# Optimization experiments

Hardware: AMD Instinct MI355X
Metric: run time of the kernel (lower is better)

The kernel has to match this reference:

```python
import jax, jax.numpy as jnp
import numpy as np

B, S, D = 2, 1024, 4096
HQ, HKV, HD = 32, 8, 128
GROUPS = HQ // HKV          # 4
SCALE = HD ** -0.5


def _rope_tables(key):
    # standard RoPE cos/sin tables, non-interleaved (half-split) layout
    inv_freq = 1.0 / (10000.0 ** (jnp.arange(0, HD, 2, dtype=jnp.float32) / HD))  # [HD/2]
    pos = jnp.arange(S, dtype=jnp.float32)                                        # [S]
    freqs = pos[:, None] * inv_freq[None, :]                                      # [S, HD/2]
    emb = jnp.concatenate([freqs, freqs], axis=-1)                                # [S, HD]
    cos = jnp.broadcast_to(jnp.cos(emb)[None], (B, S, HD))
    sin = jnp.broadcast_to(jnp.sin(emb)[None], (B, S, HD))
    return cos, sin


def setup_inputs() -> dict:
    key = jax.random.key(0)
    ks = jax.random.split(key, 6)
    hidden_states = jax.random.normal(ks[0], (B, S, D), dtype=jnp.float32)
    cos_table, sin_table = _rope_tables(ks[1])
    Wq = jax.random.normal(ks[2], (D, HQ * HD), dtype=jnp.float32) * (D ** -0.5)
    Wk = jax.random.normal(ks[3], (D, HKV * HD), dtype=jnp.float32) * (D ** -0.5)
    Wv = jax.random.normal(ks[4], (D, HKV * HD), dtype=jnp.float32) * (D ** -0.5)
    Wo = jax.random.normal(ks[5], (HQ * HD, D), dtype=jnp.float32) * ((HQ * HD) ** -0.5)
    return {"hidden_states": hidden_states, "cos_table": cos_table,
            "sin_table": sin_table, "Wq": Wq, "Wk": Wk, "Wv": Wv, "Wo": Wo}


def _rotate_half(x):
    x1, x2 = jnp.split(x, 2, axis=-1)
    return jnp.concatenate([-x2, x1], axis=-1)


def _apply_rope(x, cos, sin):
    # x: [B, S, H, HD]; cos/sin: [B, S, HD] broadcast across heads
    c = cos[:, :, None, :]
    s = sin[:, :, None, :]
    return x * c + _rotate_half(x) * s


def reference(hidden_states, cos_table, sin_table, Wq, Wk, Wv, Wo):
    b, s, _ = hidden_states.shape
    # QKV projections (no bias, Llama-style)
    q = (hidden_states @ Wq).reshape(b, s, HQ, HD)
    k = (hidden_states @ Wk).reshape(b, s, HKV, HD)
    v = (hidden_states @ Wv).reshape(b, s, HKV, HD)
    # fused RoPE on q and k (in [B, S, H, HD] layout, as in source)
    q = _apply_rope(q, cos_table, sin_table)
    k = _apply_rope(k, cos_table, sin_table)
    # -> [B, H, S, HD]
    q = q.transpose(0, 2, 1, 3)
    k = k.transpose(0, 2, 1, 3)
    v = v.transpose(0, 2, 1, 3)
    # GQA repeat_kv: [B, HKV, S, HD] -> [B, HQ, S, HD]
    k = jnp.repeat(k, GROUPS, axis=1)
    v = jnp.repeat(v, GROUPS, axis=1)
    # SDPA, no mask (source calls sdpa without a mask)
    scores = jnp.einsum('bhqd,bhkd->bhqk', q, k) * SCALE
    attn = jax.nn.softmax(scores, axis=-1)
    out = jnp.einsum('bhqk,bhkd->bhqd', attn, v)
    out = out.transpose(0, 2, 1, 3).reshape(b, s, HQ * HD)
    return out @ Wo
```

## Files before the change

kernel.cpp:

```cpp
#include <hip/hip_runtime.h>

#define B_   2
#define S_   1024
#define D_   4096
#define HQ_  32
#define HKV_ 8
#define HD_  128
#define SCALE_ 0.08838834764831845f

typedef unsigned short u16;
typedef __attribute__((ext_vector_type(8))) short s16x8;
typedef __attribute__((ext_vector_type(4))) short s16x4;
typedef __attribute__((ext_vector_type(4))) float f32x4;

#define MFMA(a,b,c) __builtin_amdgcn_mfma_f32_16x16x32_bf16((a),(b),(c),0,0,0)

__device__ __forceinline__ u16 bf16_rne(float x) {
  unsigned u = __float_as_uint(x);
  u += 0x7fffu + ((u >> 16) & 1u);
  return (u16)(u >> 16);
}
__device__ __forceinline__ float bf16_up(u16 h) {
  return __uint_as_float(((unsigned)h) << 16);
}
__device__ __forceinline__ void split2(float x, u16& h, u16& l) {
  h = bf16_rne(x);
  l = bf16_rne(x - bf16_up(h));
}

__device__ __forceinline__ void cvt_hi_lo(float a, float b, unsigned& hi, unsigned& lo) {
  unsigned h, l;
  asm("v_cvt_pk_bf16_f32 %0, %1, %2" : "=v"(h) : "v"(a), "v"(b));
  float ra = __uint_as_float(h << 16);
  float rb = __uint_as_float(h & 0xffff0000u);
  float la = a - ra, lb = b - rb;
  asm("v_cvt_pk_bf16_f32 %0, %1, %2" : "=v"(l) : "v"(la), "v"(lb));
  hi = h; lo = l;
}
__device__ __forceinline__ void pack8(float4 x, float4 y, uint4& h, uint4& l) {
  unsigned h0,h1,h2,h3,l0,l1,l2,l3;
  cvt_hi_lo(x.x, x.y, h0, l0);
  cvt_hi_lo(x.z, x.w, h1, l1);
  cvt_hi_lo(y.x, y.y, h2, l2);
  cvt_hi_lo(y.z, y.w, h3, l3);
  h = make_uint4(h0,h1,h2,h3); l = make_uint4(l0,l1,l2,l3);
}

typedef const __attribute__((address_space(1))) void* gas_ptr;
typedef __attribute__((address_space(3))) void* las_ptr;
__device__ __forceinline__ void gload_lds16(const void* g, void* l) {
  __builtin_amdgcn_global_load_lds((gas_ptr)g, (las_ptr)l, 16, 0, 0);
}

__global__ __launch_bounds__(256) void frag_b1(
    const float* __restrict__ W, u16* __restrict__ dh, u16* __restrict__ dl,
    int N, int n0, int Nc16)
{
  __shared__ float T[32][68];
  const int kt = blockIdx.x, nbk = blockIdx.y;
  const int tid = threadIdx.x;
#pragma unroll
  for (int rep = 0; rep < 2; ++rep) {
    int idx = tid + rep * 256;
    int row = idx >> 4, c4 = (idx & 15) * 4;
    float4 v = *reinterpret_cast<const float4*>(&W[(size_t)(kt*32 + row) * N + n0 + nbk*64 + c4]);
    *reinterpret_cast<float4*>(&T[row][c4]) = v;
  }
  __syncthreads();
  const size_t base = ((size_t)kt * Nc16 + nbk * 4) * 512;
  int c = tid;
  int nt = c >> 6, l = c & 63, kc = l >> 4, r = l & 15;
  u16 hh[8], ll[8];
#pragma unroll
  for (int j = 0; j < 8; ++j) split2(T[kc*8 + j][nt*16 + r], hh[j], ll[j]);
  *reinterpret_cast<s16x8*>(&dh[base + (size_t)c * 8]) =
    (s16x8){(short)hh[0],(short)hh[1],(short)hh[2],(short)hh[3],
            (short)hh[4],(short)hh[5],(short)hh[6],(short)hh[7]};
  *reinterpret_cast<s16x8*>(&dl[base + (size_t)c * 8]) =
    (s16x8){(short)ll[0],(short)ll[1],(short)ll[2],(short)ll[3],
            (short)ll[4],(short)ll[5],(short)ll[6],(short)ll[7]};
}

__global__ __launch_bounds__(256) void frag_b2(
    const float* __restrict__ W, u16* __restrict__ dh, u16* __restrict__ dl,
    int N, int n0, int Nc16)
{
  __shared__ float T[32][68];
  const int kt = blockIdx.x, nbk = blockIdx.y;
  const int tid = threadIdx.x;
#pragma unroll
  for (int rep = 0; rep < 2; ++rep) {
    int idx = tid + rep * 256;
    int row = idx >> 4, c4 = (idx & 15) * 4;
    float4 v = *reinterpret_cast<const float4*>(&W[(size_t)(kt*32 + row) * N + n0 + nbk*64 + c4]);
    *reinterpret_cast<float4*>(&T[row][c4]) = v;
  }
  __syncthreads();
  int c = tid;
  int nt = c >> 6, l = c & 63;
  const size_t base = (((size_t)(kt >> 1) * Nc16 + nbk*4 + nt) * 2 + (kt & 1)) * 512;
  u16 hh[8], ll[8];
#pragma unroll
  for (int j = 0; j < 8; ++j) split2(T[(l >> 4)*8 + j][nt*16 + (l & 15)], hh[j], ll[j]);
  *reinterpret_cast<s16x8*>(&dh[base + (size_t)l * 8]) =
    (s16x8){(short)hh[0],(short)hh[1],(short)hh[2],(short)hh[3],
            (short)hh[4],(short)hh[5],(short)hh[6],(short)hh[7]};
  *reinterpret_cast<s16x8*>(&dl[base + (size_t)l * 8]) =
    (s16x8){(short)ll[0],(short)ll[1],(short)ll[2],(short)ll[3],
            (short)ll[4],(short)ll[5],(short)ll[6],(short)ll[7]};
}

__global__ __launch_bounds__(256) void frag_a(
    const float* __restrict__ src, u16* __restrict__ dh, u16* __restrict__ dl)
{
  __shared__ float T[128][68];
  const int kt = blockIdx.x;
  const int mb = blockIdx.y;
  const int tid = threadIdx.x;
#pragma unroll
  for (int rep = 0; rep < 8; ++rep) {
    int idx = tid + rep * 256;
    int row = idx >> 4, c4 = (idx & 15) * 4;
    float4 v = *reinterpret_cast<const float4*>(&src[(size_t)(mb*128 + row) * 4096 + kt*64 + c4]);
    *reinterpret_cast<float4*>(&T[row][c4]) = v;
  }
  __syncthreads();
#pragma unroll
  for (int rep = 0; rep < 4; ++rep) {
    int c = tid + rep * 256;
    int mt = c >> 7, rem = c & 127, kk = rem >> 6, l = rem & 63;
    u16 hh[8], ll[8];
#pragma unroll
    for (int j = 0; j < 8; ++j)
      split2(T[mt*16 + (l & 15)][kk*32 + (l >> 4)*8 + j], hh[j], ll[j]);
    size_t off = (((size_t)(kt*128 + mb*8 + mt)) * 2 + kk) * 512 + (size_t)l * 8;
    *reinterpret_cast<s16x8*>(&dh[off]) =
      (s16x8){(short)hh[0],(short)hh[1],(short)hh[2],(short)hh[3],
              (short)hh[4],(short)hh[5],(short)hh[6],(short)hh[7]};
    *reinterpret_cast<s16x8*>(&dl[off]) =
      (s16x8){(short)ll[0],(short)ll[1],(short)ll[2],(short)ll[3],
              (short)ll[4],(short)ll[5],(short)ll[6],(short)ll[7]};
  }
}

__device__ __forceinline__ void gemm256_core(
    const u16* __restrict__ PAh, const u16* __restrict__ PAl,
    const u16* __restrict__ PBh, const u16* __restrict__ PBl,
    float* __restrict__ C, int ldc, int Nc16,
    int mb, int nb, int vk0, int nvk, u16* L)
{
  const int tid  = threadIdx.x;
  const int lane = tid & 63;
  const int wid  = tid >> 6;
  const int loff = lane * 8;
  const int wm8  = (wid >> 2) * 8;
  const int wn4  = (wid & 3) * 4;

  f32x4 acc[8][4];
#pragma unroll
  for (int i = 0; i < 8; ++i)
#pragma unroll
    for (int j = 0; j < 4; ++j) acc[i][j] = (f32x4){0.f,0.f,0.f,0.f};

  const size_t aBase = (size_t)mb * 16384;
  const size_t bBase = (size_t)nb * 16384;

#define STAGE256(v, la_, lb_)                                                  \
  {                                                                            \
    int p_ = (v) >> 6, vk_ = (v) & 63;                                         \
    const u16* sa_ = ((p_ == 1) ? PAl : PAh) + (size_t)vk_ * 131072 + aBase;   \
    const u16* sb_ = ((p_ == 2) ? PBl : PBh) + (size_t)vk_ * ((size_t)Nc16 * 1024) + bBase; \
    _Pragma("unroll")                                                          \
    for (int s_ = 0; s_ < 4; ++s_) {                                           \
      int ch_ = wid * 4 + s_;                                                  \
      gload_lds16(sa_ + ch_*512 + loff, (la_) + ch_*512);                      \
      gload_lds16(sb_ + ch_*512 + loff, (lb_) + ch_*512);                      \
    }                                                                          \
  }

  {
    u16* la = L + ((vk0 & 1) ? 16384 : 0);
    u16* lb = L + 32768 + ((vk0 & 1) ? 16384 : 0);
    STAGE256(vk0, la, lb);
  }
  __syncthreads();

  for (int t = vk0; t < vk0 + nvk; ++t) {
    u16* la = L + ((t & 1) ? 16384 : 0);
    u16* lb = L + 32768 + ((t & 1) ? 16384 : 0);
    if (t + 1 < vk0 + nvk) {
      u16* na = L + (((t+1) & 1) ? 16384 : 0);
      u16* nbuf = L + 32768 + (((t+1) & 1) ? 16384 : 0);
      STAGE256(t+1, na, nbuf);
    }
#pragma unroll
    for (int kk = 0; kk < 2; ++kk) {
      s16x8 a[8];
#pragma unroll
      for (int mf = 0; mf < 8; ++mf)
        a[mf] = *reinterpret_cast<const s16x8*>(&la[((wm8+mf)*2 + kk)*512 + loff]);
      __builtin_amdgcn_s_setprio(1);
#pragma unroll
      for (int nf = 0; nf < 4; ++nf) {
        s16x8 b = *reinterpret_cast<const s16x8*>(&lb[((wn4+nf)*2 + kk)*512 + loff]);
#pragma unroll
        for (int mf = 0; mf < 8; ++mf)
          acc[mf][nf] = MFMA(a[mf], b, acc[mf][nf]);
      }
      __builtin_amdgcn_s_setprio(0);
    }
    __syncthreads();
  }
#undef STAGE256

  const int lg = lane >> 4, lr = lane & 15;
  const int row0 = mb*256 + (wid >> 2) * 128;
  const int col0 = nb*256 + (wid & 3) * 64;
#pragma unroll
  for (int mf = 0; mf < 8; ++mf)
#pragma unroll
    for (int nf = 0; nf < 4; ++nf)
#pragma unroll
      for (int r = 0; r < 4; ++r)
        C[(size_t)(row0 + mf*16 + lg*4 + r) * ldc + col0 + nf*16 + lr] = acc[mf][nf][r];
}

__global__ __launch_bounds__(512) void gemm_qkv2(
    const u16* __restrict__ XAh, const u16* __restrict__ XAl,
    const u16* __restrict__ WA,
    float* __restrict__ qb, float* __restrict__ kb, float* __restrict__ vb)
{
  __shared__ __attribute__((aligned(16))) u16 L[65536];
  int id = blockIdx.x;
  int swz = (id & 7) * 24 + (id >> 3);
  const u16 *Bh, *Bl; float* C; int ldc, Nc16, mb, nb;
  if (swz < 128)      { Bh = WA;          Bl = WA+16777216; C = qb; ldc = 4096; Nc16 = 256; mb = swz & 7;  nb = swz >> 3; }
  else if (swz < 160) { int u = swz-128; Bh = WA+33554432; Bl = WA+37748736; C = kb; ldc = 1024; Nc16 = 64; mb = u & 7; nb = u >> 3; }
  else                { int u = swz-160; Bh = WA+41943040; Bl = WA+46137344; C = vb; ldc = 1024; Nc16 = 64; mb = u & 7; nb = u >> 3; }
  gemm256_core(XAh, XAl, Bh, Bl, C, ldc, Nc16, mb, nb, 0, 192, L);
}

__global__ __launch_bounds__(512) void gemm_out2(
    const u16* __restrict__ ABh, const u16* __restrict__ ABl,
    const u16* __restrict__ WOh, const u16* __restrict__ WOl,
    float* __restrict__ outp, float* __restrict__ c2)
{
  __shared__ __attribute__((aligned(16))) u16 L[65536];
  int id = blockIdx.x;
  int swz = (id & 7) * 32 + (id >> 3);
  int u = swz & 127, s = swz >> 7;
  int mb = u & 7, nb = u >> 3;
  gemm256_core(ABh, ABl, WOh, WOl, s ? c2 : outp, 4096, 256, mb, nb, s*96, 96, L);
}

__global__ __launch_bounds__(256) void add_out(
    float* __restrict__ o, const float* __restrict__ c2)
{
  int i = blockIdx.x * 256 + threadIdx.x;
  float4 a = reinterpret_cast<float4*>(o)[i];
  float4 b = reinterpret_cast<const float4*>(c2)[i];
  a.x += b.x; a.y += b.y; a.z += b.z; a.w += b.w;
  reinterpret_cast<float4*>(o)[i] = a;
}

__global__ __launch_bounds__(256) void frag_kv(
    const float* __restrict__ kb, const float* __restrict__ vb,
    const float* __restrict__ cosT, const float* __restrict__ sinT,
    u16* __restrict__ KFh, u16* __restrict__ KFl,
    u16* __restrict__ VFh, u16* __restrict__ VFl)
{
  __shared__ float T[32][132];
  const int bid  = blockIdx.x;
  const int isV  = bid >> 9;
  const int bkvh = (bid >> 5) & 15;
  const int chnk = bid & 31;
  const int tid  = threadIdx.x;
  const int b    = bkvh >> 3, kvh = bkvh & 7;

  const float* src = isV ? vb : kb;
  {
    int r0 = tid >> 5, c4 = (tid & 31) * 4;
    float sgn = (c4 < 64) ? -1.f : 1.f;
#pragma unroll
    for (int it = 0; it < 4; ++it) {
      int row = r0 + it * 8;
      int srow = chnk*32 + row;
      const float* rp = &src[(((size_t)(b * S_ + srow)) * HKV_ + kvh) * HD_];
      float4 v = *reinterpret_cast<const float4*>(rp + c4);
      if (!isV) {
        float4 p  = *reinterpret_cast<const float4*>(rp + (c4 ^ 64));
        float4 cc = *reinterpret_cast<const float4*>(&cosT[((size_t)(b*S_ + srow))*HD_ + c4]);
        float4 ss = *reinterpret_cast<const float4*>(&sinT[((size_t)(b*S_ + srow))*HD_ + c4]);
        v.x = v.x*cc.x + sgn*p.x*ss.x;
        v.y = v.y*cc.y + sgn*p.y*ss.y;
        v.z = v.z*cc.z + sgn*p.z*ss.z;
        v.w = v.w*cc.w + sgn*p.w*ss.w;
      }
      *reinterpret_cast<float4*>(&T[row][c4]) = v;
    }
  }
  __syncthreads();
#pragma unroll
  for (int rep = 0; rep < 2; ++rep) {
    int c2 = tid + rep * 256;
    int l = c2 & 63;
    u16 hh[8], ll[8];
    if (!isV) {
      int f = c2 >> 6, st_loc = f >> 2, dt = f & 3;
#pragma unroll
      for (int j = 0; j < 8; ++j)
        split2(T[st_loc*16 + (l & 15)][dt*32 + (l >> 4)*8 + j], hh[j], ll[j]);
      size_t off = ((size_t)bkvh*64 + chnk*2) * 2048 + (size_t)c2 * 8;
      *reinterpret_cast<s16x8*>(&KFh[off]) =
        (s16x8){(short)hh[0],(short)hh[1],(short)hh[2],(short)hh[3],
                (short)hh[4],(short)hh[5],(short)hh[6],(short)hh[7]};
      *reinterpret_cast<s16x8*>(&KFl[off]) =
        (s16x8){(short)ll[0],(short)ll[1],(short)ll[2],(short)ll[3],
                (short)ll[4],(short)ll[5],(short)ll[6],(short)ll[7]};
    } else {
      int dt16 = c2 >> 6;
#pragma unroll
      for (int j = 0; j < 8; ++j)
        split2(T[(l >> 4)*8 + j][dt16*16 + (l & 15)], hh[j], ll[j]);
      size_t off = ((size_t)bkvh*32 + chnk) * 4096 + (size_t)c2 * 8;
      *reinterpret_cast<s16x8*>(&VFh[off]) =
        (s16x8){(short)hh[0],(short)hh[1],(short)hh[2],(short)hh[3],
                (short)hh[4],(short)hh[5],(short)hh[6],(short)hh[7]};
      *reinterpret_cast<s16x8*>(&VFl[off]) =
        (s16x8){(short)ll[0],(short)ll[1],(short)ll[2],(short)ll[3],
                (short)ll[4],(short)ll[5],(short)ll[6],(short)ll[7]};
    }
  }
}

__global__ __launch_bounds__(512) void attn3(
    const float* __restrict__ qb,
    const float* __restrict__ cosT, const float* __restrict__ sinT,
    const u16* __restrict__ KFh, const u16* __restrict__ KFl,
    const u16* __restrict__ VFh, const u16* __restrict__ VFl,
    float* __restrict__ ob)
{
  __shared__ __attribute__((aligned(16))) u16 Klds[16384];
  __shared__ __attribute__((aligned(16))) u16 Vlds[16384];
  __shared__ u16 Ph[8][16][68], Pl[8][16][68];

  const int tid  = threadIdx.x;
  const int lane = tid & 63;
  const int wid  = tid >> 6;
  const int lr   = lane & 15;
  const int lg   = lane >> 4;
  const int loff = lane * 8;
  const int qt   = blockIdx.x;
  const int bh   = blockIdx.y;
  const int b    = bh >> 5, h = bh & 31;
  const int bkvh = b * 8 + (h >> 2);

  s16x8 qh[4], ql[4];
  {
    const int qrow = qt * 128 + wid * 16 + lr;
    const float* qp = qb + ((size_t)((b * S_ + qrow) * HQ_ + h)) * HD_;
    const float* cp = cosT + ((size_t)(b * S_ + qrow)) * HD_;
    const float* sp = sinT + ((size_t)(b * S_ + qrow)) * HD_;
#pragma unroll
    for (int kc = 0; kc < 4; ++kc) {
      const int d0 = kc * 32 + lg * 8;
      const float sgn = (d0 < 64) ? -1.f : 1.f;
      float4 v0 = *reinterpret_cast<const float4*>(qp + d0);
      float4 v1 = *reinterpret_cast<const float4*>(qp + d0 + 4);
      float4 p0 = *reinterpret_cast<const float4*>(qp + (d0 ^ 64));
      float4 p1 = *reinterpret_cast<const float4*>(qp + (d0 ^ 64) + 4);
      float4 c0 = *reinterpret_cast<const float4*>(cp + d0);
      float4 c1 = *reinterpret_cast<const float4*>(cp + d0 + 4);
      float4 s0 = *reinterpret_cast<const float4*>(sp + d0);
      float4 s1 = *reinterpret_cast<const float4*>(sp + d0 + 4);
      float4 r0, r1;
      r0.x = v0.x*c0.x + sgn*p0.x*s0.x;  r0.y = v0.y*c0.y + sgn*p0.y*s0.y;
      r0.z = v0.z*c0.z + sgn*p0.z*s0.z;  r0.w = v0.w*c0.w + sgn*p0.w*s0.w;
      r1.x = v1.x*c1.x + sgn*p1.x*s1.x;  r1.y = v1.y*c1.y + sgn*p1.y*s1.y;
      r1.z = v1.z*c1.z + sgn*p1.z*s1.z;  r1.w = v1.w*c1.w + sgn*p1.w*s1.w;
      uint4 h4, l4; pack8(r0, r1, h4, l4);
      qh[kc] = *reinterpret_cast<s16x8*>(&h4);
      ql[kc] = *reinterpret_cast<s16x8*>(&l4);
    }
  }

  f32x4 acc_o[8];
#pragma unroll
  for (int df = 0; df < 8; ++df) acc_o[df] = (f32x4){0.f, 0.f, 0.f, 0.f};
  float m_run[4] = {-1e30f, -1e30f, -1e30f, -1e30f};
  float l_run[4] = {0.f, 0.f, 0.f, 0.f};

  const u16* gKh = KFh + (size_t)bkvh * 131072;
  const u16* gKl = KFl + (size_t)bkvh * 131072;
  const u16* gVh = VFh + (size_t)bkvh * 131072;
  const u16* gVl = VFl + (size_t)bkvh * 131072;

#pragma unroll
  for (int i = 0; i < 4; ++i) {
    int idx = wid * 4 + i;
    const u16* src = (idx < 16) ? (gKh + idx*512) : (gKl + (idx-16)*512);
    u16* dst = Klds + ((idx < 16) ? idx*512 : 8192 + (idx-16)*512);
    gload_lds16(src + loff, dst);
  }
  __syncthreads();

  for (int t = 0; t < 16; ++t) {
#pragma unroll
    for (int i = 0; i < 4; ++i) {
      int idx = wid * 4 + i;
      const u16* src = (idx < 16) ? (gVh + t*8192 + idx*512)
                                  : (gVl + t*8192 + (idx-16)*512);
      u16* dst = Vlds + ((idx < 16) ? idx*512 : 8192 + (idx-16)*512);
      gload_lds16(src + loff, dst);
    }

    f32x4 accs[4];
#pragma unroll
    for (int nf = 0; nf < 4; ++nf) {
      accs[nf] = (f32x4){0.f, 0.f, 0.f, 0.f};
      s16x8 kh8[4], kl8[4];
#pragma unroll
      for (int kc = 0; kc < 4; ++kc) {
        kh8[kc] = *reinterpret_cast<const s16x8*>(&Klds[nf*2048 + kc*512 + loff]);
        kl8[kc] = *reinterpret_cast<const s16x8*>(&Klds[8192 + nf*2048 + kc*512 + loff]);
      }
#pragma unroll
      for (int kc = 0; kc < 4; ++kc) {
        accs[nf] = MFMA(qh[kc], kh8[kc], accs[nf]);
        accs[nf] = MFMA(ql[kc], kh8[kc], accs[nf]);
        accs[nf] = MFMA(qh[kc], kl8[kc], accs[nf]);
      }
    }
#pragma unroll
    for (int nf = 0; nf < 4; ++nf) accs[nf] *= SCALE_;

    float corr[4], rsum[4];
#pragma unroll
    for (int r = 0; r < 4; ++r) {
      float t0 = fmaxf(fmaxf(accs[0][r], accs[1][r]), fmaxf(accs[2][r], accs[3][r]));
      t0 = fmaxf(t0, __shfl_xor(t0, 1));
      t0 = fmaxf(t0, __shfl_xor(t0, 2));
      t0 = fmaxf(t0, __shfl_xor(t0, 4));
      t0 = fmaxf(t0, __shfl_xor(t0, 8));
      float mnew = fmaxf(m_run[r], t0);
      corr[r] = __expf(m_run[r] - mnew);
      m_run[r] = mnew;
      rsum[r] = 0.f;
    }
#pragma unroll
    for (int nf = 0; nf < 4; ++nf)
#pragma unroll
      for (int r = 0; r < 4; ++r) {
        float p = __expf(accs[nf][r] - m_run[r]);
        rsum[r] += p;
        u16 ph, pl;
        split2(p, ph, pl);
        Ph[wid][lg*4 + r][nf*16 + lr] = ph;
        Pl[wid][lg*4 + r][nf*16 + lr] = pl;
      }
#pragma unroll
    for (int r = 0; r < 4; ++r) {
      float s = rsum[r];
      s += __shfl_xor(s, 1); s += __shfl_xor(s, 2);
      s += __shfl_xor(s, 4); s += __shfl_xor(s, 8);
      l_run[r] = l_run[r] * corr[r] + s;
    }
#pragma unroll
    for (int df = 0; df < 8; ++df)
#pragma unroll
      for (int r = 0; r < 4; ++r) acc_o[df][r] *= corr[r];

    __syncthreads();

    if (t < 15) {
#pragma unroll
      for (int i = 0; i < 4; ++i) {
        int idx = wid * 4 + i;
        const u16* src = (idx < 16) ? (gKh + (t+1)*8192 + idx*512)
                                    : (gKl + (t+1)*8192 + (idx-16)*512);
        u16* dst = Klds + ((idx < 16) ? idx*512 : 8192 + (idx-16)*512);
        gload_lds16(src + loff, dst);
      }
    }

    s16x8 pa_h[2], pa_l[2];
#pragma unroll
    for (int kc = 0; kc < 2; ++kc) {
      pa_h[kc] = *reinterpret_cast<const s16x8*>(&Ph[wid][lr][kc*32 + lg*8]);
      pa_l[kc] = *reinterpret_cast<const s16x8*>(&Pl[wid][lr][kc*32 + lg*8]);
    }
#pragma unroll
    for (int df = 0; df < 8; ++df) {
      s16x8 vh8[2], vl8[2];
#pragma unroll
      for (int kc = 0; kc < 2; ++kc) {
        vh8[kc] = *reinterpret_cast<const s16x8*>(&Vlds[kc*4096 + df*512 + loff]);
        vl8[kc] = *reinterpret_cast<const s16x8*>(&Vlds[8192 + kc*4096 + df*512 + loff]);
      }
#pragma unroll
      for (int kc = 0; kc < 2; ++kc) {
        acc_o[df] = MFMA(pa_h[kc], vh8[kc], acc_o[df]);
        acc_o[df] = MFMA(pa_l[kc], vh8[kc], acc_o[df]);
        acc_o[df] = MFMA(pa_h[kc], vl8[kc], acc_o[df]);
      }
    }
    __syncthreads();
  }

  float inv_l[4];
#pragma unroll
  for (int r = 0; r < 4; ++r) inv_l[r] = 1.f / l_run[r];
#pragma unroll
  for (int df = 0; df < 8; ++df)
#pragma unroll
    for (int r = 0; r < 4; ++r) {
      int row = qt * 128 + wid * 16 + lg * 4 + r;
      ob[((size_t)((b * S_ + row) * HQ_ + h)) * HD_ + df*16 + lr] = acc_o[df][r] * inv_l[r];
    }
}

__global__ __launch_bounds__(512) void gemm_p1(
    const float* __restrict__ X, const float* __restrict__ abp,
    const u16* __restrict__ WF,
    float* __restrict__ qb, float* __restrict__ kb, float* __restrict__ vb,
    float* __restrict__ outp, int mode, int col0)
{
  __shared__ __attribute__((aligned(16))) u16 lds[40960];
  u16* ah0 = lds;
  u16* al0 = lds + 4096;
  u16* ah1 = lds + 8192;
  u16* al1 = lds + 12288;
  u16* bh0 = lds + 16384;
  u16* bh1 = lds + 24576;
  u16* blb = lds + 32768;

  const int id   = blockIdx.x;
  const int cpx  = gridDim.x >> 3;
  const int swz  = (id & 7) * cpx + (id >> 3);

  const float* A; const u16* Bh; const u16* Bl; float* C;
  int ldc, Nc16, mb, nb;
  if (mode == 3) {
    A=abp; Bh=WF; Bl=WF+16777216; C=outp; ldc=4096; Nc16=256; mb=swz>>4; nb=swz&15;
  } else {
    if (swz < 128)      { A=X; Bh=WF;          Bl=WF+8388608;  C=qb;      ldc=4096; Nc16=128; mb=swz>>3; nb=swz&7; }
    else if (swz < 256) { int u=swz-128; A=X; Bh=WF+16777216; Bl=WF+25165824; C=qb+2048; ldc=4096; Nc16=128; mb=u>>3; nb=u&7; }
    else if (swz < 320) { int u=swz-256; A=X; Bh=WF+33554432; Bl=WF+37748736; C=kb; ldc=1024; Nc16=64; mb=u>>2; nb=u&3; }
    else                { int u=swz-320; A=X; Bh=WF+41943040; Bl=WF+46137344; C=vb; ldc=1024; Nc16=64; mb=u>>2; nb=u&3; }
  }

  const int tid  = threadIdx.x;
  const int lane = tid & 63;
  const int wid  = tid >> 6;
  const int mtb  = (wid >> 2) * 4;
  const int ntb  = (wid & 3) * 4;
  const int loff = lane * 8;
  const int lg   = lane >> 4;
  const int lr_  = lane & 15;
  const int aoff = (lg*16 + ((lr_ + 4*lg) & 15)) * 8;

  const int arow = tid >> 2;
  const int akc  = tid & 3;
  const float* aptr = A + (size_t)(mb*128 + arow) * 4096 + akc*8;
  const int awr = (arow >> 4)*512 + (akc*16 + (((arow & 15) + 4*akc) & 15))*8;

  const size_t bStep = (size_t)Nc16 * 512;
  const u16* pBh = Bh + (size_t)nb*16*512 + loff;
  const u16* pBl = Bl + (size_t)nb*16*512 + loff;

  f32x4 acc[4][4];
#pragma unroll
  for (int i = 0; i < 4; ++i)
#pragma unroll
    for (int j = 0; j < 4; ++j) acc[i][j] = (f32x4){0.f, 0.f, 0.f, 0.f};

  float4 ra0 = *reinterpret_cast<const float4*>(aptr);
  float4 ra1 = *reinterpret_cast<const float4*>(aptr + 4);
  {
    uint4 h4, l4; pack8(ra0, ra1, h4, l4);
    *reinterpret_cast<uint4*>(&ah0[awr]) = h4;
    *reinterpret_cast<uint4*>(&al0[awr]) = l4;
  }
  gload_lds16(pBh + (size_t)wid*512,     bh0 + wid*512);
  gload_lds16(pBh + (size_t)(wid+8)*512, bh0 + (wid+8)*512);
  ra0 = *reinterpret_cast<const float4*>(aptr + 32);
  ra1 = *reinterpret_cast<const float4*>(aptr + 36);
  __syncthreads();

  for (int kt = 0; kt < 128; ++kt) {
    u16* cAh = (kt & 1) ? ah1 : ah0;
    u16* cAl = (kt & 1) ? al1 : al0;
    u16* nAh = (kt & 1) ? ah0 : ah1;
    u16* nAl = (kt & 1) ? al0 : al1;
    u16* cBh = (kt & 1) ? bh1 : bh0;
    u16* nBh = (kt & 1) ? bh0 : bh1;

    gload_lds16(pBl + (size_t)kt*bStep + (size_t)wid*512,     blb + wid*512);
    gload_lds16(pBl + (size_t)kt*bStep + (size_t)(wid+8)*512, blb + (wid+8)*512);
    if (kt < 127) {
      gload_lds16(pBh + (size_t)(kt+1)*bStep + (size_t)wid*512,     nBh + wid*512);
      gload_lds16(pBh + (size_t)(kt+1)*bStep + (size_t)(wid+8)*512, nBh + (wid+8)*512);
    }
    s16x8 a_h[4], a_l[4], b_h[4];
#pragma unroll
    for (int mf = 0; mf < 4; ++mf) {
      a_h[mf] = *reinterpret_cast<const s16x8*>(&cAh[(mtb+mf)*512 + aoff]);
      a_l[mf] = *reinterpret_cast<const s16x8*>(&cAl[(mtb+mf)*512 + aoff]);
    }
#pragma unroll
    for (int nf = 0; nf < 4; ++nf)
      b_h[nf] = *reinterpret_cast<const s16x8*>(&cBh[(ntb+nf)*512 + loff]);
#pragma unroll
    for (int mf = 0; mf < 4; ++mf)
#pragma unroll
      for (int nf = 0; nf < 4; ++nf) {
        acc[mf][nf] = MFMA(a_h[mf], b_h[nf], acc[mf][nf]);
        acc[mf][nf] = MFMA(a_l[mf], b_h[nf], acc[mf][nf]);
      }
    __syncthreads();

    s16x8 b_l[4];
#pragma unroll
    for (int nf = 0; nf < 4; ++nf)
      b_l[nf] = *reinterpret_cast<const s16x8*>(&blb[(ntb+nf)*512 + loff]);
#pragma unroll
    for (int mf = 0; mf < 4; ++mf)
#pragma unroll
      for (int nf = 0; nf < 4; ++nf)
        acc[mf][nf] = MFMA(a_h[mf], b_l[nf], acc[mf][nf]);
    if (kt < 127) {
      uint4 h4, l4; pack8(ra0, ra1, h4, l4);
      *reinterpret_cast<uint4*>(&nAh[awr]) = h4;
      *reinterpret_cast<uint4*>(&nAl[awr]) = l4;
      if (kt < 126) {
        ra0 = *reinterpret_cast<const float4*>(aptr + (kt+2)*32);
        ra1 = *reinterpret_cast<const float4*>(aptr + (kt+2)*32 + 4);
      }
    }
    __syncthreads();
  }

  const int row0 = mb*128 + (wid >> 2) * 64;
  const int nloc = nb*256 + (wid & 3) * 64;
#pragma unroll
  for (int mf = 0; mf < 4; ++mf)
#pragma unroll
    for (int nf = 0; nf < 4; ++nf)
#pragma unroll
      for (int r = 0; r < 4; ++r)
        C[(size_t)(row0 + mf*16 + lg*4 + r) * ldc + nloc + nf*16 + lr_] = acc[mf][nf][r];
}

extern "C" void kernel_launch(void* const* d_in, const int* in_sizes, int n_in,
                              void* d_out, int out_size, void* d_ws, size_t ws_size,
                              hipStream_t stream)
{
  const float* hs   = (const float*)d_in[0];
  const float* cosT = (const float*)d_in[1];
  const float* sinT = (const float*)d_in[2];
  const float* Wq   = (const float*)d_in[3];
  const float* Wk   = (const float*)d_in[4];
  const float* Wv   = (const float*)d_in[5];
  const float* Wo   = (const float*)d_in[6];
  float* out = (float*)d_out;

  float* qb = (float*)d_ws;
  float* kb = qb + 8388608;
  float* vb = kb + 2097152;
  float* ab = vb + 2097152;
  u16*   FR = (u16*)(ab + 8388608);

  const size_t WS208 = 218103808ULL;
  const size_t WS185 = 184549376ULL;

  if (ws_size >= WS208) {
    u16* XAh = FR;
    u16* XAl = FR + 8388608;
    u16* WA  = FR + 16777216;
    frag_a<<<dim3(64,16), 256, 0, stream>>>(hs, XAh, XAl);
    frag_b2<<<dim3(128,64), 256, 0, stream>>>(Wq, WA,           WA+16777216, 4096, 0, 256);
    frag_b2<<<dim3(128,16), 256, 0, stream>>>(Wk, WA+33554432,  WA+37748736, 1024, 0, 64);
    frag_b2<<<dim3(128,16), 256, 0, stream>>>(Wv, WA+41943040,  WA+46137344, 1024, 0, 64);
    gemm_qkv2<<<192, 512, 0, stream>>>(XAh, XAl, WA, qb, kb, vb);
    frag_kv<<<1024, 256, 0, stream>>>(kb, vb, cosT, sinT,
                                      WA, WA+2097152, WA+4194304, WA+6291456);
    frag_b2<<<dim3(128,64), 256, 0, stream>>>(Wo, WA+8388608, WA+25165824, 4096, 0, 256);
    attn3<<<dim3(8, 64), 512, 0, stream>>>(qb, cosT, sinT,
                                           WA, WA+2097152, WA+4194304, WA+6291456, ab);
    frag_a<<<dim3(64,16), 256, 0, stream>>>(ab, XAh, XAl);
    gemm_out2<<<256, 512, 0, stream>>>(XAh, XAl, WA+8388608, WA+25165824, out, qb);
    add_out<<<8192, 256, 0, stream>>>(out, qb);
  } else {
    u16* WF = FR;
    u16* KFh = WF;
    u16* KFl = WF + 2097152;
    u16* VFh = WF + 4194304;
    u16* VFl = WF + 6291456;
    frag_b1<<<dim3(128,32), 256, 0, stream>>>(Wq, WF,          WF+8388608,  4096, 0,    128);
    frag_b1<<<dim3(128,32), 256, 0, stream>>>(Wq, WF+16777216, WF+25165824, 4096, 2048, 128);
    frag_b1<<<dim3(128,16), 256, 0, stream>>>(Wk, WF+33554432, WF+37748736, 1024, 0,    64);
    frag_b1<<<dim3(128,16), 256, 0, stream>>>(Wv, WF+41943040, WF+46137344, 1024, 0,    64);
    gemm_p1<<<384, 512, 0, stream>>>(hs, ab, WF, qb, kb, vb, out, 5, 0);
    frag_kv<<<1024, 256, 0, stream>>>(kb, vb, cosT, sinT, KFh, KFl, VFh, VFl);
    attn3<<<dim3(8, 64), 512, 0, stream>>>(qb, cosT, sinT, KFh, KFl, VFh, VFl, ab);
    frag_b1<<<dim3(128,64), 256, 0, stream>>>(Wo, WF, WF+16777216, 4096, 0, 256);
    gemm_p1<<<256, 512, 0, stream>>>(hs, ab, WF, qb, kb, vb, out, 3, 0);
  }
}
```

Baseline: 698.2 us.

## Fuse Q/K/V weights into one interleaved B matrix with 256x192 GEMM tiles

```diff
diff --git a/kernel.cpp b/kernel.cpp
--- a/kernel.cpp
+++ b/kernel.cpp
@@ -52,9 +52,9 @@
   __builtin_amdgcn_global_load_lds((gas_ptr)g, (las_ptr)l, 16, 0, 0);
 }
 
-__global__ __launch_bounds__(256) void frag_b1(
+__global__ __launch_bounds__(256) void frag_b2(
     const float* __restrict__ W, u16* __restrict__ dh, u16* __restrict__ dl,
-    int N, int n0, int Nc16)
+    int N, int n0, int Ntot16, int ntoff)
 {
   __shared__ float T[32][68];
   const int kt = blockIdx.x, nbk = blockIdx.y;
@@ -67,38 +67,9 @@
     *reinterpret_cast<float4*>(&T[row][c4]) = v;
   }
   __syncthreads();
-  const size_t base = ((size_t)kt * Nc16 + nbk * 4) * 512;
-  int c = tid;
-  int nt = c >> 6, l = c & 63, kc = l >> 4, r = l & 15;
-  u16 hh[8], ll[8];
-#pragma unroll
-  for (int j = 0; j < 8; ++j) split2(T[kc*8 + j][nt*16 + r], hh[j], ll[j]);
-  *reinterpret_cast<s16x8*>(&dh[base + (size_t)c * 8]) =
-    (s16x8){(short)hh[0],(short)hh[1],(short)hh[2],(short)hh[3],
-            (short)hh[4],(short)hh[5],(short)hh[6],(short)hh[7]};
-  *reinterpret_cast<s16x8*>(&dl[base + (size_t)c * 8]) =
-    (s16x8){(short)ll[0],(short)ll[1],(short)ll[2],(short)ll[3],
-            (short)ll[4],(short)ll[5],(short)ll[6],(short)ll[7]};
-}
-
-__global__ __launch_bounds__(256) void frag_b2(
-    const float* __restrict__ W, u16* __restrict__ dh, u16* __restrict__ dl,
-    int N, int n0, int Nc16)
-{
-  __shared__ float T[32][68];
-  const int kt = blockIdx.x, nbk = blockIdx.y;
-  const int tid = threadIdx.x;
-#pragma unroll
-  for (int rep = 0; rep < 2; ++rep) {
-    int idx = tid + rep * 256;
-    int row = idx >> 4, c4 = (idx & 15) * 4;
-    float4 v = *reinterpret_cast<const float4*>(&W[(size_t)(kt*32 + row) * N + n0 + nbk*64 + c4]);
-    *reinterpret_cast<float4*>(&T[row][c4]) = v;
-  }
-  __syncthreads();
   int c = tid;
   int nt = c >> 6, l = c & 63;
-  const size_t base = (((size_t)(kt >> 1) * Nc16 + nbk*4 + nt) * 2 + (kt & 1)) * 512;
+  const size_t base = (((size_t)(kt >> 1) * Ntot16 + ntoff + nbk*4 + nt) * 2 + (kt & 1)) * 512;
   u16 hh[8], ll[8];
 #pragma unroll
   for (int j = 0; j < 8; ++j) split2(T[(l >> 4)*8 + j][nt*16 + (l & 15)], hh[j], ll[j]);
@@ -143,56 +114,55 @@
   }
 }
 
+template<int NF, bool RQ>
 __device__ __forceinline__ void gemm256_core(
     const u16* __restrict__ PAh, const u16* __restrict__ PAl,
     const u16* __restrict__ PBh, const u16* __restrict__ PBl,
-    float* __restrict__ C, int ldc, int Nc16,
-    int mb, int nb, int vk0, int nvk, u16* L)
+    float* __restrict__ C0, float* __restrict__ C1, float* __restrict__ C2,
+    int ldc0, int Nt16, int mb, int nb, int vk0, int nvk, u16* L)
 {
   const int tid  = threadIdx.x;
   const int lane = tid & 63;
   const int wid  = tid >> 6;
   const int loff = lane * 8;
   const int wm8  = (wid >> 2) * 8;
-  const int wn4  = (wid & 3) * 4;
-
-  f32x4 acc[8][4];
+  const int wnf  = (wid & 3) * NF;
+
+  u16* A0 = L;
+  u16* A1 = L + 16384;
+  u16* B0 = L + 32768;
+  u16* B1 = L + 32768 + NF*4096;
+
+  f32x4 acc[8][NF];
 #pragma unroll
   for (int i = 0; i < 8; ++i)
 #pragma unroll
-    for (int j = 0; j < 4; ++j) acc[i][j] = (f32x4){0.f,0.f,0.f,0.f};
+    for (int j = 0; j < NF; ++j) acc[i][j] = (f32x4){0.f,0.f,0.f,0.f};
 
   const size_t aBase = (size_t)mb * 16384;
-  const size_t bBase = (size_t)nb * 16384;
-
-#define STAGE256(v, la_, lb_)                                                  \
-  {                                                                            \
-    int p_ = (v) >> 6, vk_ = (v) & 63;                                         \
-    const u16* sa_ = ((p_ == 1) ? PAl : PAh) + (size_t)vk_ * 131072 + aBase;   \
-    const u16* sb_ = ((p_ == 2) ? PBl : PBh) + (size_t)vk_ * ((size_t)Nc16 * 1024) + bBase; \
-    _Pragma("unroll")                                                          \
-    for (int s_ = 0; s_ < 4; ++s_) {                                           \
-      int ch_ = wid * 4 + s_;                                                  \
-      gload_lds16(sa_ + ch_*512 + loff, (la_) + ch_*512);                      \
-      gload_lds16(sb_ + ch_*512 + loff, (lb_) + ch_*512);                      \
-    }                                                                          \
-  }
-
-  {
-    u16* la = L + ((vk0 & 1) ? 16384 : 0);
-    u16* lb = L + 32768 + ((vk0 & 1) ? 16384 : 0);
-    STAGE256(vk0, la, lb);
-  }
+  const size_t bBase = (size_t)nb * (NF * 4096);
+  const size_t bSlab = (size_t)Nt16 * 1024;
+
+  auto STAGE = [&](int v, u16* la_, u16* lb_) {
+    int p = v >> 6, k = v & 63;
+    const u16* sa = ((p == 1) ? PAl : PAh) + (size_t)k * 131072 + aBase + loff;
+    const u16* sb = ((p == 2) ? PBl : PBh) + (size_t)k * bSlab + bBase + loff;
+#pragma unroll
+    for (int s = 0; s < 4; ++s)
+      gload_lds16(sa + (wid*4 + s)*512, la_ + (wid*4 + s)*512);
+#pragma unroll
+    for (int s = 0; s < NF; ++s)
+      gload_lds16(sb + (wid*NF + s)*512, lb_ + (wid*NF + s)*512);
+  };
+
+  STAGE(vk0, (vk0 & 1) ? A1 : A0, (vk0 & 1) ? B1 : B0);
   __syncthreads();
 
   for (int t = vk0; t < vk0 + nvk; ++t) {
-    u16* la = L + ((t & 1) ? 16384 : 0);
-    u16* lb = L + 32768 + ((t & 1) ? 16384 : 0);
-    if (t + 1 < vk0 + nvk) {
-      u16* na = L + (((t+1) & 1) ? 16384 : 0);
-      u16* nbuf = L + 32768 + (((t+1) & 1) ? 16384 : 0);
-      STAGE256(t+1, na, nbuf);
-    }
+    u16* la = (t & 1) ? A1 : A0;
+    u16* lb = (t & 1) ? B1 : B0;
+    if (t + 1 < vk0 + nvk)
+      STAGE(t + 1, (t & 1) ? A0 : A1, (t & 1) ? B0 : B1);
 #pragma unroll
     for (int kk = 0; kk < 2; ++kk) {
       s16x8 a[8];
@@ -201,8 +171,8 @@
         a[mf] = *reinterpret_cast<const s16x8*>(&la[((wm8+mf)*2 + kk)*512 + loff]);
       __builtin_amdgcn_s_setprio(1);
 #pragma unroll
-      for (int nf = 0; nf < 4; ++nf) {
-        s16x8 b = *reinterpret_cast<const s16x8*>(&lb[((wn4+nf)*2 + kk)*512 + loff]);
+      for (int nf = 0; nf < NF; ++nf) {
+        s16x8 b = *reinterpret_cast<const s16x8*>(&lb[((wnf+nf)*2 + kk)*512 + loff]);
 #pragma unroll
         for (int mf = 0; mf < 8; ++mf)
           acc[mf][nf] = MFMA(a[mf], b, acc[mf][nf]);
@@ -211,18 +181,39 @@
     }
     __syncthreads();
   }
-#undef STAGE256
 
   const int lg = lane >> 4, lr = lane & 15;
-  const int row0 = mb*256 + (wid >> 2) * 128;
-  const int col0 = nb*256 + (wid & 3) * 64;
+  const int rowb = mb*256 + (wid >> 2) * 128;
 #pragma unroll
   for (int mf = 0; mf < 8; ++mf)
 #pragma unroll
-    for (int nf = 0; nf < 4; ++nf)
-#pragma unroll
-      for (int r = 0; r < 4; ++r)
-        C[(size_t)(row0 + mf*16 + lg*4 + r) * ldc + col0 + nf*16 + lr] = acc[mf][nf][r];
+    for (int nf = 0; nf < NF; ++nf)
+#pragma unroll
+      for (int r = 0; r < 4; ++r) {
+        int row = rowb + mf*16 + lg*4 + r;
+        float v = acc[mf][nf][r];
+        if constexpr (RQ) {
+          int gcol = nb*(NF*64) + (wid & 3)*(NF*16) + nf*16 + lr;
+          if (gcol < 4096)      C0[(size_t)row * 4096 + gcol] = v;
+          else if (gcol < 5120) C1[(size_t)row * 1024 + (gcol - 4096)] = v;
+          else                  C2[(size_t)row * 1024 + (gcol - 5120)] = v;
+        } else {
+          int col = nb*(NF*64) + (wid & 3)*(NF*16) + nf*16 + lr;
+          C0[(size_t)row * ldc0 + col] = v;
+        }
+      }
+}
+
+__global__ __launch_bounds__(512) void gemm_qkv3(
+    const u16* __restrict__ XAh, const u16* __restrict__ XAl,
+    const u16* __restrict__ WBh, const u16* __restrict__ WBl,
+    float* __restrict__ qb, float* __restrict__ kb, float* __restrict__ vb)
+{
+  __shared__ __attribute__((aligned(16))) u16 L[57344];
+  int id = blockIdx.x;
+  int swz = (id & 7) * 32 + (id >> 3);
+  int mb = swz >> 5, nb = swz & 31;
+  gemm256_core<3, true>(XAh, XAl, WBh, WBl, qb, kb, vb, 0, 384, mb, nb, 0, 192, L);
 }
 
 __global__ __launch_bounds__(512) void gemm_qkv2(
@@ -233,11 +224,11 @@
   __shared__ __attribute__((aligned(16))) u16 L[65536];
   int id = blockIdx.x;
   int swz = (id & 7) * 24 + (id >> 3);
-  const u16 *Bh, *Bl; float* C; int ldc, Nc16, mb, nb;
-  if (swz < 128)      { Bh = WA;          Bl = WA+16777216; C = qb; ldc = 4096; Nc16 = 256; mb = swz & 7;  nb = swz >> 3; }
-  else if (swz < 160) { int u = swz-128; Bh = WA+33554432; Bl = WA+37748736; C = kb; ldc = 1024; Nc16 = 64; mb = u & 7; nb = u >> 3; }
-  else                { int u = swz-160; Bh = WA+41943040; Bl = WA+46137344; C = vb; ldc = 1024; Nc16 = 64; mb = u & 7; nb = u >> 3; }
-  gemm256_core(XAh, XAl, Bh, Bl, C, ldc, Nc16, mb, nb, 0, 192, L);
+  const u16 *Bh, *Bl; float* C; int ldc, Nt16, mb, nb;
+  if (swz < 128)      { Bh = WA;          Bl = WA+16777216; C = qb; ldc = 4096; Nt16 = 256; mb = swz & 7;  nb = swz >> 3; }
+  else if (swz < 160) { int u = swz-128; Bh = WA+33554432; Bl = WA+37748736; C = kb; ldc = 1024; Nt16 = 64; mb = u & 7; nb = u >> 3; }
+  else                { int u = swz-160; Bh = WA+41943040; Bl = WA+46137344; C = vb; ldc = 1024; Nt16 = 64; mb = u & 7; nb = u >> 3; }
+  gemm256_core<4, false>(XAh, XAl, Bh, Bl, C, nullptr, nullptr, ldc, Nt16, mb, nb, 0, 192, L);
 }
 
 __global__ __launch_bounds__(512) void gemm_out2(
@@ -250,7 +241,8 @@
   int swz = (id & 7) * 32 + (id >> 3);
   int u = swz & 127, s = swz >> 7;
   int mb = u & 7, nb = u >> 3;
-  gemm256_core(ABh, ABl, WOh, WOl, s ? c2 : outp, 4096, 256, mb, nb, s*96, 96, L);
+  gemm256_core<4, false>(ABh, ABl, WOh, WOl, s ? c2 : outp, nullptr, nullptr,
+                         4096, 256, mb, nb, s*96, 96, L);
 }
 
 __global__ __launch_bounds__(256) void add_out(
@@ -519,138 +511,6 @@
     }
 }
 
-__global__ __launch_bounds__(512) void gemm_p1(
-    const float* __restrict__ X, const float* __restrict__ abp,
-    const u16* __restrict__ WF,
-    float* __restrict__ qb, float* __restrict__ kb, float* __restrict__ vb,
-    float* __restrict__ outp, int mode, int col0)
-{
-  __shared__ __attribute__((aligned(16))) u16 lds[40960];
-  u16* ah0 = lds;
-  u16* al0 = lds + 4096;
-  u16* ah1 = lds + 8192;
-  u16* al1 = lds + 12288;
-  u16* bh0 = lds + 16384;
-  u16* bh1 = lds + 24576;
-  u16* blb = lds + 32768;
-
-  const int id   = blockIdx.x;
-  const int cpx  = gridDim.x >> 3;
-  const int swz  = (id & 7) * cpx + (id >> 3);
-
-  const float* A; const u16* Bh; const u16* Bl; float* C;
-  int ldc, Nc16, mb, nb;
-  if (mode == 3) {
-    A=abp; Bh=WF; Bl=WF+16777216; C=outp; ldc=4096; Nc16=256; mb=swz>>4; nb=swz&15;
-  } else {
-    if (swz < 128)      { A=X; Bh=WF;          Bl=WF+8388608;  C=qb;      ldc=4096; Nc16=128; mb=swz>>3; nb=swz&7; }
-    else if (swz < 256) { int u=swz-128; A=X; Bh=WF+16777216; Bl=WF+25165824; C=qb+2048; ldc=4096; Nc16=128; mb=u>>3; nb=u&7; }
-    else if (swz < 320) { int u=swz-256; A=X; Bh=WF+33554432; Bl=WF+37748736; C=kb; ldc=1024; Nc16=64; mb=u>>2; nb=u&3; }
-    else                { int u=swz-320; A=X; Bh=WF+41943040; Bl=WF+46137344; C=vb; ldc=1024; Nc16=64; mb=u>>2; nb=u&3; }
-  }
-
-  const int tid  = threadIdx.x;
-  const int lane = tid & 63;
-  const int wid  = tid >> 6;
-  const int mtb  = (wid >> 2) * 4;
-  const int ntb  = (wid & 3) * 4;
-  const int loff = lane * 8;
-  const int lg   = lane >> 4;
-  const int lr_  = lane & 15;
-  const int aoff = (lg*16 + ((lr_ + 4*lg) & 15)) * 8;
-
-  const int arow = tid >> 2;
-  const int akc  = tid & 3;
-  const float* aptr = A + (size_t)(mb*128 + arow) * 4096 + akc*8;
-  const int awr = (arow >> 4)*512 + (akc*16 + (((arow & 15) + 4*akc) & 15))*8;
-
-  const size_t bStep = (size_t)Nc16 * 512;
-  const u16* pBh = Bh + (size_t)nb*16*512 + loff;
-  const u16* pBl = Bl + (size_t)nb*16*512 + loff;
-
-  f32x4 acc[4][4];
-#pragma unroll
-  for (int i = 0; i < 4; ++i)
-#pragma unroll
-    for (int j = 0; j < 4; ++j) acc[i][j] = (f32x4){0.f, 0.f, 0.f, 0.f};
-
-  float4 ra0 = *reinterpret_cast<const float4*>(aptr);
-  float4 ra1 = *reinterpret_cast<const float4*>(aptr + 4);
-  {
-    uint4 h4, l4; pack8(ra0, ra1, h4, l4);
-    *reinterpret_cast<uint4*>(&ah0[awr]) = h4;
-    *reinterpret_cast<uint4*>(&al0[awr]) = l4;
-  }
-  gload_lds16(pBh + (size_t)wid*512,     bh0 + wid*512);
-  gload_lds16(pBh + (size_t)(wid+8)*512, bh0 + (wid+8)*512);
-  ra0 = *reinterpret_cast<const float4*>(aptr + 32);
-  ra1 = *reinterpret_cast<const float4*>(aptr + 36);
-  __syncthreads();
-
-  for (int kt = 0; kt < 128; ++kt) {
-    u16* cAh = (kt & 1) ? ah1 : ah0;
-    u16* cAl = (kt & 1) ? al1 : al0;
-    u16* nAh = (kt & 1) ? ah0 : ah1;
-    u16* nAl = (kt & 1) ? al0 : al1;
-    u16* cBh = (kt & 1) ? bh1 : bh0;
-    u16* nBh = (kt & 1) ? bh0 : bh1;
-
-    gload_lds16(pBl + (size_t)kt*bStep + (size_t)wid*512,     blb + wid*512);
-    gload_lds16(pBl + (size_t)kt*bStep + (size_t)(wid+8)*512, blb + (wid+8)*512);
-    if (kt < 127) {
-      gload_lds16(pBh + (size_t)(kt+1)*bStep + (size_t)wid*512,     nBh + wid*512);
-      gload_lds16(pBh + (size_t)(kt+1)*bStep + (size_t)(wid+8)*512, nBh + (wid+8)*512);
-    }
-    s16x8 a_h[4], a_l[4], b_h[4];
-#pragma unroll
-    for (int mf = 0; mf < 4; ++mf) {
-      a_h[mf] = *reinterpret_cast<const s16x8*>(&cAh[(mtb+mf)*512 + aoff]);
-      a_l[mf] = *reinterpret_cast<const s16x8*>(&cAl[(mtb+mf)*512 + aoff]);
-    }
-#pragma unroll
-    for (int nf = 0; nf < 4; ++nf)
-      b_h[nf] = *reinterpret_cast<const s16x8*>(&cBh[(ntb+nf)*512 + loff]);
-#pragma unroll
-    for (int mf = 0; mf < 4; ++mf)
-#pragma unroll
-      for (int nf = 0; nf < 4; ++nf) {
-        acc[mf][nf] = MFMA(a_h[mf], b_h[nf], acc[mf][nf]);
-        acc[mf][nf] = MFMA(a_l[mf], b_h[nf], acc[mf][nf]);
-      }
-    __syncthreads();
-
-    s16x8 b_l[4];
-#pragma unroll
-    for (int nf = 0; nf < 4; ++nf)
-      b_l[nf] = *reinterpret_cast<const s16x8*>(&blb[(ntb+nf)*512 + loff]);
-#pragma unroll
-    for (int mf = 0; mf < 4; ++mf)
-#pragma unroll
-      for (int nf = 0; nf < 4; ++nf)
-        acc[mf][nf] = MFMA(a_h[mf], b_l[nf], acc[mf][nf]);
-    if (kt < 127) {
-      uint4 h4, l4; pack8(ra0, ra1, h4, l4);
-      *reinterpret_cast<uint4*>(&nAh[awr]) = h4;
-      *reinterpret_cast<uint4*>(&nAl[awr]) = l4;
-      if (kt < 126) {
-        ra0 = *reinterpret_cast<const float4*>(aptr + (kt+2)*32);
-        ra1 = *reinterpret_cast<const float4*>(aptr + (kt+2)*32 + 4);
-      }
-    }
-    __syncthreads();
-  }
-
-  const int row0 = mb*128 + (wid >> 2) * 64;
-  const int nloc = nb*256 + (wid & 3) * 64;
-#pragma unroll
-  for (int mf = 0; mf < 4; ++mf)
-#pragma unroll
-    for (int nf = 0; nf < 4; ++nf)
-#pragma unroll
-      for (int r = 0; r < 4; ++r)
-        C[(size_t)(row0 + mf*16 + lg*4 + r) * ldc + nloc + nf*16 + lr_] = acc[mf][nf][r];
-}
-
 extern "C" void kernel_launch(void* const* d_in, const int* in_sizes, int n_in,
                               void* d_out, int out_size, void* d_ws, size_t ws_size,
                               hipStream_t stream)
@@ -670,40 +530,48 @@
   float* ab = vb + 2097152;
   u16*   FR = (u16*)(ab + 8388608);
 
+  const size_t WS212 = 222298112ULL;
   const size_t WS208 = 218103808ULL;
-  const size_t WS185 = 184549376ULL;
-
-  if (ws_size >= WS208) {
+
+  if (ws_size >= WS212) {
+    u16* XAh = FR;
+    u16* XAl = FR + 8388608;
+    u16* WBh = FR + 16777216;
+    u16* WBl = FR + 41943040;
+    u16* KFh = FR + 16777216;
+    u16* KFl = FR + 18874368;
+    u16* VFh = FR + 20971520;
+    u16* VFl = FR + 23068672;
+    u16* WOh = FR + 25165824;
+    u16* WOl = FR + 41943040;
+
+    frag_a<<<dim3(64,16), 256, 0, stream>>>(hs, XAh, XAl);
+    frag_b2<<<dim3(128,64), 256, 0, stream>>>(Wq, WBh, WBl, 4096, 0, 384, 0);
+    frag_b2<<<dim3(128,16), 256, 0, stream>>>(Wk, WBh, WBl, 1024, 0, 384, 256);
+    frag_b2<<<dim3(128,16), 256, 0, stream>>>(Wv, WBh, WBl, 1024, 0, 384, 320);
+    gemm_qkv3<<<256, 512, 0, stream>>>(XAh, XAl, WBh, WBl, qb, kb, vb);
+    frag_kv<<<1024, 256, 0, stream>>>(kb, vb, cosT, sinT, KFh, KFl, VFh, VFl);
+    frag_b2<<<dim3(128,64), 256, 0, stream>>>(Wo, WOh, WOl, 4096, 0, 256, 0);
+    attn3<<<dim3(8, 64), 512, 0, stream>>>(qb, cosT, sinT, KFh, KFl, VFh, VFl, ab);
+    frag_a<<<dim3(64,16), 256, 0, stream>>>(ab, XAh, XAl);
+    gemm_out2<<<256, 512, 0, stream>>>(XAh, XAl, WOh, WOl, out, qb);
+    add_out<<<8192, 256, 0, stream>>>(out, qb);
+  } else {
     u16* XAh = FR;
     u16* XAl = FR + 8388608;
     u16* WA  = FR + 16777216;
     frag_a<<<dim3(64,16), 256, 0, stream>>>(hs, XAh, XAl);
-    frag_b2<<<dim3(128,64), 256, 0, stream>>>(Wq, WA,           WA+16777216, 4096, 0, 256);
-    frag_b2<<<dim3(128,16), 256, 0, stream>>>(Wk, WA+33554432,  WA+37748736, 1024, 0, 64);
-    frag_b2<<<dim3(128,16), 256, 0, stream>>>(Wv, WA+41943040,  WA+46137344, 1024, 0, 64);
+    frag_b2<<<dim3(128,64), 256, 0, stream>>>(Wq, WA,           WA+16777216, 4096, 0, 256, 0);
+    frag_b2<<<dim3(128,16), 256, 0, stream>>>(Wk, WA+33554432,  WA+37748736, 1024, 0, 64, 0);
+    frag_b2<<<dim3(128,16), 256, 0, stream>>>(Wv, WA+41943040,  WA+46137344, 1024, 0, 64, 0);
     gemm_qkv2<<<192, 512, 0, stream>>>(XAh, XAl, WA, qb, kb, vb);
     frag_kv<<<1024, 256, 0, stream>>>(kb, vb, cosT, sinT,
                                       WA, WA+2097152, WA+4194304, WA+6291456);
-    frag_b2<<<dim3(128,64), 256, 0, stream>>>(Wo, WA+8388608, WA+25165824, 4096, 0, 256);
+    frag_b2<<<dim3(128,64), 256, 0, stream>>>(Wo, WA+8388608, WA+25165824, 4096, 0, 256, 0);
     attn3<<<dim3(8, 64), 512, 0, stream>>>(qb, cosT, sinT,
                                            WA, WA+2097152, WA+4194304, WA+6291456, ab);
     frag_a<<<dim3(64,16), 256, 0, stream>>>(ab, XAh, XAl);
     gemm_out2<<<256, 512, 0, stream>>>(XAh, XAl, WA+8388608, WA+25165824, out, qb);
     add_out<<<8192, 256, 0, stream>>>(out, qb);
-  } else {
-    u16* WF = FR;
-    u16* KFh = WF;
-    u16* KFl = WF + 2097152;
-    u16* VFh = WF + 4194304;
-    u16* VFl = WF + 6291456;
-    frag_b1<<<dim3(128,32), 256, 0, stream>>>(Wq, WF,          WF+8388608,  4096, 0,    128);
-    frag_b1<<<dim3(128,32), 256, 0, stream>>>(Wq, WF+16777216, WF+25165824, 4096, 2048, 128);
-    frag_b1<<<dim3(128,16), 256, 0, stream>>>(Wk, WF+33554432, WF+37748736, 1024, 0,    64);
-    frag_b1<<<dim3(128,16), 256, 0, stream>>>(Wv, WF+41943040, WF+46137344, 1024, 0,    64);
-    gemm_p1<<<384, 512, 0, stream>>>(hs, ab, WF, qb, kb, vb, out, 5, 0);
-    frag_kv<<<1024, 256, 0, stream>>>(kb, vb, cosT, sinT, KFh, KFl, VFh, VFl);
-    attn3<<<dim3(8, 64), 512, 0, stream>>>(qb, cosT, sinT, KFh, KFl, VFh, VFl, ab);
-    frag_b1<<<dim3(128,64), 256, 0, stream>>>(Wo, WF, WF+16777216, 4096, 0, 256);
-    gemm_p1<<<256, 512, 0, stream>>>(hs, ab, WF, qb, kb, vb, out, 3, 0);
-  }
-}
+  }
+}
```

After: 690.5 us. Within noise of the previous version (-1.1%).
